# Performance work log

Measured on AMD Instinct MI355X. Metric: run time of the kernel, lower is better.

The kernel has to match this reference:

```python
import jax, jax.numpy as jnp
import numpy as np

N, F, B, H = 4096, 64, 16, 8  # nodes, feat dim, graphs, GAT heads


def _graph():
    # symmetric random graph (avg deg ~8), plus exact 2-hop and 3-hop edge lists
    # (this reproduces torch_sparse.spspmm with coalesced=True on the boolean structure)
    rng = np.random.default_rng(0)
    s = rng.integers(0, N, 8192)
    d = rng.integers(0, N, 8192)
    m = s != d
    s, d = s[m], d[m]
    rows = np.concatenate([s, d]).astype(np.int64)
    cols = np.concatenate([d, s]).astype(np.int64)
    key = np.unique(rows * N + cols)
    rows, cols = key // N, key % N
    A = np.zeros((N, N), np.float32)
    A[rows, cols] = 1.0
    A2 = (A @ A) > 0
    A3 = (A2.astype(np.float32) @ A) > 0
    np.fill_diagonal(A2, False)  # GATConv/GCNConv remove then re-add self-loops
    np.fill_diagonal(A3, False)
    e1 = np.stack([rows, cols]).astype(np.int64)
    e2 = np.stack(np.nonzero(A2)).astype(np.int64)
    e3 = np.stack(np.nonzero(A3)).astype(np.int64)
    return e1, e2, e3


def _sl(ei, n):
    loops = jnp.arange(n, dtype=ei.dtype)
    return jnp.concatenate([ei, jnp.stack([loops, loops])], axis=1)


def _seg_softmax(logits, seg, n):
    m = jax.ops.segment_max(logits, seg, num_segments=n)
    e = jnp.exp(logits - m[seg])
    s = jax.ops.segment_sum(e, seg, num_segments=n)
    return e / s[seg]


def _gat(x, ei, W, a_src, a_dst, b, heads):
    # PyG GATConv: per-head linear, edge attention logits, softmax over incoming edges
    n = x.shape[0]
    d = a_src.shape[1]
    h = (x @ W).reshape(n, heads, d)  # [N,H,D]
    src, dst = ei[0], ei[1]
    al = jnp.einsum('nhd,hd->nh', h, a_src)
    ar = jnp.einsum('nhd,hd->nh', h, a_dst)
    logit = jax.nn.leaky_relu(al[src] + ar[dst], 0.2)  # [E,H]
    alpha = _seg_softmax(logit, dst, n)
    out = jax.ops.segment_sum(alpha[:, :, None] * h[src], dst, num_segments=n)
    return out.reshape(n, heads * d) + b


def _gcn(x, ei, W, b):
    n = x.shape[0]
    src, dst = ei[0], ei[1]
    h = x @ W
    deg = jax.ops.segment_sum(jnp.ones(src.shape, x.dtype), dst, num_segments=n)
    dinv = jnp.where(deg > 0, deg ** -0.5, 0.0)
    norm = dinv[src] * dinv[dst]
    return jax.ops.segment_sum(norm[:, None] * h[src], dst, num_segments=n) + b


def setup_inputs():
    key = jax.random.key(0)
    ks = iter(jax.random.split(key, 40))
    e1, e2, e3 = _graph()
    p = lambda *shape: jax.random.normal(next(ks), shape, jnp.float32) * 0.1
    return dict(
        x=jax.random.normal(next(ks), (N, F), jnp.float32),
        edge_index=jnp.asarray(e1), edge_index2=jnp.asarray(e2), edge_index3=jnp.asarray(e3),
        batch=jnp.asarray(np.repeat(np.arange(B), N // B)),
        g1_W=p(F, H * F), g1_as=p(H, F), g1_ad=p(H, F), g1_b=p(H * F),
        g2_W=p(H * F, F), g2_as=p(1, F), g2_ad=p(1, F), g2_b=p(F),
        gfc_W=p(F, F), gfc_b=p(F), gfc1_W=p(F, 128), gfc1_b=p(128),
        gout_W=p(128, F), gout_b=p(F),
        c2_W=p(F, 2 * F), c2_b=p(2 * F), c3_W=p(2 * F, 4 * F), c3_b=p(4 * F),
        A_W=p(4 * F, F), A_b=p(F), B_W=p(2 * F, F), B_b=p(F),
        Wih=p(F, 3 * F), Whh=p(F, 3 * F), bih=p(3 * F), bhh=p(3 * F),
        f1_W=p(F, 128), f1_b=p(128), f2_W=p(128, 120), f2_b=p(120),
    )


def reference(x, edge_index, edge_index2, edge_index3, batch,
              g1_W, g1_as, g1_ad, g1_b, g2_W, g2_as, g2_ad, g2_b,
              gfc_W, gfc_b, gfc1_W, gfc1_b, gout_W, gout_b,
              c2_W, c2_b, c3_W, c3_b, A_W, A_b, B_W, B_b,
              Wih, Whh, bih, bhh, f1_W, f1_b, f2_W, f2_b):
    n = x.shape[0]
    e1, e2, e3 = _sl(edge_index, n), _sl(edge_index2, n), _sl(edge_index3, n)

    def gat_block(xin, ei):  # inner GAT module (eval mode: dropouts are identity)
        h = jax.nn.elu(_gat(xin, ei, g1_W, g1_as, g1_ad, g1_b, H))
        h = jax.nn.relu(_gat(h, ei, g2_W, g2_as, g2_ad, g2_b, 1))
        h = jax.nn.relu(h @ gfc_W + gfc_b)
        h = jax.nn.relu(h @ gfc1_W + gfc1_b)
        return h @ gout_W + gout_b

    h1 = jax.nn.relu(gat_block(x, e1))
    h2 = jax.nn.relu(_gcn(h1, e1, c2_W, c2_b))
    h3 = jax.nn.relu(_gcn(h2, e1, c3_W, c3_b))            # [N,4F]
    h4 = jax.nn.relu(gat_block(x, e2))
    h5 = jax.nn.relu(_gcn(h4, e2, c2_W, c2_b))            # [N,2F]
    h6 = jax.nn.relu(gat_block(x, e3))                     # [N,F]

    # GateUpdate
    b_ = h5 @ B_W + B_b
    a_ = h3 @ A_W + A_b
    z = jax.nn.sigmoid(a_ + b_)
    hg = z * b_ + (1 - z) * a_
    # GRUCell(h6, hg)
    gi = h6 @ Wih + bih
    gh = hg @ Whh + bhh
    r = jax.nn.sigmoid(gi[:, :F] + gh[:, :F])
    zz = jax.nn.sigmoid(gi[:, F:2 * F] + gh[:, F:2 * F])
    nn_ = jnp.tanh(gi[:, 2 * F:] + r * gh[:, 2 * F:])
    cc = (1 - zz) * nn_ + zz * hg

    g = jax.ops.segment_max(cc, batch, num_segments=B)    # global_max_pool -> [B,F]
    g = jax.nn.relu(g @ f1_W + f1_b)
    return g @ f2_W + f2_b                                 # [B,120]
```

## Files before the change

kernel.cpp:

```cpp
#include <hip/hip_runtime.h>
#include <math.h>

#define NN 4096
#define NG 16
#define WB() __builtin_amdgcn_wave_barrier()

__global__ void rowptr3_kernel(const int* __restrict__ ea, int Ea,
                               const int* __restrict__ eb, int Eb,
                               const int* __restrict__ ec, int Ec,
                               int* __restrict__ rpa, int* __restrict__ rpb, int* __restrict__ rpc){
    int t = blockIdx.x * blockDim.x + threadIdx.x;
    int set = t / (NN + 1), i = t % (NN + 1);
    if (set >= 3) return;
    const int* e0 = set == 0 ? ea : set == 1 ? eb : ec;
    int E        = set == 0 ? Ea : set == 1 ? Eb : Ec;
    int* rp      = set == 0 ? rpa : set == 1 ? rpb : rpc;
    if (i == NN){ rp[NN] = E; return; }
    int lo = 0, hi = E;
    while (lo < hi){ int mid = (lo + hi) >> 1; if (e0[mid] < i) lo = mid + 1; else hi = mid; }
    rp[i] = lo;
}

__global__ void dinv2_kernel(const int* __restrict__ rp1, const int* __restrict__ rp2,
                             float* __restrict__ dinv1, float* __restrict__ dinv2){
    int t = blockIdx.x * blockDim.x + threadIdx.x;
    int set = t >> 12, i = t & (NN - 1);
    if (set >= 2) return;
    const int* rp = set ? rp2 : rp1;
    float deg = (float)(rp[i+1] - rp[i] + 1);
    (set ? dinv2 : dinv1)[i] = 1.0f / sqrtf(deg);
}

__global__ __launch_bounds__(256)
void gemm_kernel(const float* __restrict__ A, const float* __restrict__ W,
                 const float* __restrict__ bias, float* __restrict__ C,
                 int K, int Nc, int act){
    __shared__ float As[64][17];
    __shared__ float Bs[16][64];
    const int tid = threadIdx.x;
    const int tx = tid & 15, ty = tid >> 4;
    const int row0 = blockIdx.y * 64, col0 = blockIdx.x * 64;
    float acc[4][4] = {};
    for (int k0 = 0; k0 < K; k0 += 16){
        {   int idx = tid * 4; int r = idx >> 4, kk = idx & 15;
            float4 av = *reinterpret_cast<const float4*>(&A[(size_t)(row0 + r) * K + k0 + kk]);
            As[r][kk+0]=av.x; As[r][kk+1]=av.y; As[r][kk+2]=av.z; As[r][kk+3]=av.w; }
        {   int idx = tid * 4; int r = idx >> 6, cc = idx & 63;
            float4 wv = *reinterpret_cast<const float4*>(&W[(size_t)(k0 + r) * Nc + col0 + cc]);
            *reinterpret_cast<float4*>(&Bs[r][cc]) = wv; }
        __syncthreads();
        #pragma unroll
        for (int kk = 0; kk < 16; ++kk){
            float a[4], b[4];
            #pragma unroll
            for (int i = 0; i < 4; ++i) a[i] = As[ty*4+i][kk];
            #pragma unroll
            for (int j = 0; j < 4; ++j) b[j] = Bs[kk][tx*4+j];
            #pragma unroll
            for (int i = 0; i < 4; ++i)
                #pragma unroll
                for (int j = 0; j < 4; ++j) acc[i][j] += a[i]*b[j];
        }
        __syncthreads();
    }
    #pragma unroll
    for (int i = 0; i < 4; ++i){
        int r = row0 + ty*4 + i;
        #pragma unroll
        for (int j = 0; j < 4; ++j){
            int c = col0 + tx*4 + j;
            float v = acc[i][j] + (bias ? bias[c] : 0.0f);
            if (act == 1) v = fmaxf(v, 0.0f);
            C[(size_t)r * Nc + c] = v;
        }
    }
}

__global__ __launch_bounds__(256)
void gemm32_kernel(const float* __restrict__ A, const float* __restrict__ W,
                   const float* __restrict__ bias, float* __restrict__ C,
                   int K, int Nc, int act){
    __shared__ float As[32][17];
    __shared__ float Bs[16][64];
    const int tid = threadIdx.x;
    const int tx = tid & 15, ty = tid >> 4;
    const int row0 = blockIdx.y * 32, col0 = blockIdx.x * 64;
    float acc[2][4] = {};
    for (int k0 = 0; k0 < K; k0 += 16){
        {   int idx = tid * 2; int r = idx >> 4, kk = idx & 15;
            float2 av = *reinterpret_cast<const float2*>(&A[(size_t)(row0 + r) * K + k0 + kk]);
            As[r][kk] = av.x; As[r][kk+1] = av.y; }
        {   int idx = tid * 4; int r = idx >> 6, cc = idx & 63;
            *reinterpret_cast<float4*>(&Bs[r][cc]) =
                *reinterpret_cast<const float4*>(&W[(size_t)(k0 + r) * Nc + col0 + cc]); }
        __syncthreads();
        #pragma unroll
        for (int kk = 0; kk < 16; ++kk){
            float a0 = As[ty*2][kk], a1 = As[ty*2+1][kk];
            float b[4];
            #pragma unroll
            for (int j = 0; j < 4; ++j) b[j] = Bs[kk][tx*4+j];
            #pragma unroll
            for (int j = 0; j < 4; ++j){ acc[0][j] += a0*b[j]; acc[1][j] += a1*b[j]; }
        }
        __syncthreads();
    }
    #pragma unroll
    for (int i = 0; i < 2; ++i){
        int r = row0 + ty*2 + i;
        #pragma unroll
        for (int j = 0; j < 4; ++j){
            int c = col0 + tx*4 + j;
            float v = acc[i][j] + (bias ? bias[c] : 0.0f);
            if (act == 1) v = fmaxf(v, 0.0f);
            C[(size_t)r * Nc + c] = v;
        }
    }
}

__global__ __launch_bounds__(256)
void attn_dot8_kernel(const float* __restrict__ h,
                      const float* __restrict__ a_src, const float* __restrict__ a_dst,
                      float* __restrict__ al, float* __restrict__ ar){
    const int lane = threadIdx.x & 63, wid = threadIdx.x >> 6;
    const int n = blockIdx.x * 4 + wid;
    float x[8], y[8];
    #pragma unroll
    for (int c = 0; c < 8; ++c){
        float v = h[(size_t)n*512 + c*64 + lane];
        x[c] = v * a_src[c*64 + lane];
        y[c] = v * a_dst[c*64 + lane];
    }
    #pragma unroll
    for (int off = 1; off < 64; off <<= 1){
        #pragma unroll
        for (int c = 0; c < 8; ++c){
            x[c] += __shfl_xor(x[c], off);
            y[c] += __shfl_xor(y[c], off);
        }
    }
    if (lane == 0){
        #pragma unroll
        for (int c = 0; c < 8; ++c){ al[n*8 + c] = x[c]; ar[n*8 + c] = y[c]; }
    }
}

__global__ __launch_bounds__(256)
void attn_dot1_kernel(const float* __restrict__ h,
                      const float* __restrict__ a_src, const float* __restrict__ a_dst,
                      float* __restrict__ al, float* __restrict__ ar){
    const int lane = threadIdx.x & 63, wid = threadIdx.x >> 6;
    const int n = blockIdx.x * 4 + wid;
    float v = h[(size_t)n*64 + lane];
    float x = v * a_src[lane], y = v * a_dst[lane];
    #pragma unroll
    for (int off = 1; off < 64; off <<= 1){ x += __shfl_xor(x, off); y += __shfl_xor(y, off); }
    if (lane == 0){ al[n] = x; ar[n] = y; }
}

__global__ __launch_bounds__(64)
void attn_ms8_kernel(const float* __restrict__ al, const float* __restrict__ ar,
                     const int* __restrict__ rpA, const int* __restrict__ rpB, const int* __restrict__ rpC,
                     const int* __restrict__ clA, const int* __restrict__ clB, const int* __restrict__ clC,
                     float* __restrict__ m8, float* __restrict__ s8){
    const int g = blockIdx.x;
    const int set = g >> 12, i = g & (NN - 1);
    const int lane = threadIdx.x;
    const int* rowptr = set == 0 ? rpA : set == 1 ? rpB : rpC;
    const int* cols   = set == 0 ? clA : set == 1 ? clB : clC;
    const int start = rowptr[i], end = rowptr[i+1];

    float al_i[8], ar_i[8];
    {
        float4 t0 = *reinterpret_cast<const float4*>(&al[(size_t)i*8]);
        float4 t1 = *reinterpret_cast<const float4*>(&al[(size_t)i*8+4]);
        al_i[0]=t0.x; al_i[1]=t0.y; al_i[2]=t0.z; al_i[3]=t0.w;
        al_i[4]=t1.x; al_i[5]=t1.y; al_i[6]=t1.z; al_i[7]=t1.w;
        float4 u0 = *reinterpret_cast<const float4*>(&ar[(size_t)i*8]);
        float4 u1 = *reinterpret_cast<const float4*>(&ar[(size_t)i*8+4]);
        ar_i[0]=u0.x; ar_i[1]=u0.y; ar_i[2]=u0.z; ar_i[3]=u0.w;
        ar_i[4]=u1.x; ar_i[5]=u1.y; ar_i[6]=u1.z; ar_i[7]=u1.w;
    }
    float m[8], s[8];
    #pragma unroll
    for (int h = 0; h < 8; ++h){ m[h] = -1e30f; s[h] = 0.f; }
    for (int k = start + lane; k < end; k += 64){
        int j = cols[k];
        float4 t0 = *reinterpret_cast<const float4*>(&al[(size_t)j*8]);
        float4 t1 = *reinterpret_cast<const float4*>(&al[(size_t)j*8+4]);
        float av[8] = {t0.x,t0.y,t0.z,t0.w,t1.x,t1.y,t1.z,t1.w};
        #pragma unroll
        for (int h = 0; h < 8; ++h){
            float x = av[h] + ar_i[h];
            x = x >= 0.f ? x : 0.2f * x;
            float mn = fmaxf(m[h], x);
            s[h] = s[h] * __expf(m[h] - mn) + __expf(x - mn);
            m[h] = mn;
        }
    }
    if (lane == 0){
        #pragma unroll
        for (int h = 0; h < 8; ++h){
            float x = al_i[h] + ar_i[h];
            x = x >= 0.f ? x : 0.2f * x;
            float mn = fmaxf(m[h], x);
            s[h] = s[h] * __expf(m[h] - mn) + __expf(x - mn);
            m[h] = mn;
        }
    }
    #pragma unroll
    for (int off = 1; off < 64; off <<= 1){
        #pragma unroll
        for (int h = 0; h < 8; ++h){
            float m2 = __shfl_xor(m[h], off), s2 = __shfl_xor(s[h], off);
            float mn = fmaxf(m[h], m2);
            s[h] = s[h] * __expf(m[h] - mn) + s2 * __expf(m2 - mn);
            m[h] = mn;
        }
    }
    if (lane == 0){
        #pragma unroll
        for (int h = 0; h < 8; ++h){ m8[(size_t)g*8 + h] = m[h]; s8[(size_t)g*8 + h] = s[h]; }
    }
}

__global__ __launch_bounds__(64)
void gat_agg8_p2_kernel(const float* __restrict__ hfeat,
                        const float* __restrict__ al, const float* __restrict__ ar,
                        const float* __restrict__ m8, const float* __restrict__ s8,
                        const int* __restrict__ rpA, const int* __restrict__ rpB, const int* __restrict__ rpC,
                        const int* __restrict__ clA, const int* __restrict__ clB, const int* __restrict__ clC,
                        const float* __restrict__ bias, float* __restrict__ out){
    const int bid = blockIdx.x;
    const int g = bid >> 1, half = bid & 1;
    const int set = g >> 12, i = g & (NN - 1);
    const int lane = threadIdx.x;
    const int* rowptr = set == 0 ? rpA : set == 1 ? rpB : rpC;
    const int* cols   = set == 0 ? clA : set == 1 ? clB : clC;
    const int start = rowptr[i], end = rowptr[i+1];
    const int deg = end - start;
    const int hb = half * 4;
    const int c0 = half * 256 + 4 * lane;
    const int hr = lane >> 4;

    float4 mv = *reinterpret_cast<const float4*>(&m8[(size_t)g*8 + hb]);
    float4 sv = *reinterpret_cast<const float4*>(&s8[(size_t)g*8 + hb]);
    float mh[4] = {mv.x, mv.y, mv.z, mv.w};
    float sh[4] = {sv.x, sv.y, sv.z, sv.w};
    float4 arv = *reinterpret_cast<const float4*>(&ar[(size_t)i*8 + hb]);
    float ar_i[4] = {arv.x, arv.y, arv.z, arv.w};
    float4 alv = *reinterpret_cast<const float4*>(&al[(size_t)i*8 + hb]);
    float al_i[4] = {alv.x, alv.y, alv.z, alv.w};

    __shared__ int   sbuf[64];
    __shared__ float wbuf[64][5];
    float4 A0 = {0.f, 0.f, 0.f, 0.f};
    for (int k0 = 0; k0 < deg; k0 += 64){
        int cnt = min(64, deg - k0);
        if (lane < cnt){
            int j = cols[start + k0 + lane];
            sbuf[lane] = j;
            float4 av = *reinterpret_cast<const float4*>(&al[(size_t)j*8 + hb]);
            float a4[4] = {av.x, av.y, av.z, av.w};
            #pragma unroll
            for (int h = 0; h < 4; ++h){
                float x = a4[h] + ar_i[h];
                x = x >= 0.f ? x : 0.2f * x;
                wbuf[lane][h] = __expf(x - mh[h]);
            }
        }
        __syncthreads();
        int e = 0;
        for (; e + 4 <= cnt; e += 4){
            int j0 = sbuf[e], j1 = sbuf[e+1], j2 = sbuf[e+2], j3 = sbuf[e+3];
            float4 v0 = *reinterpret_cast<const float4*>(&hfeat[(size_t)j0*512 + c0]);
            float4 v1 = *reinterpret_cast<const float4*>(&hfeat[(size_t)j1*512 + c0]);
            float4 v2 = *reinterpret_cast<const float4*>(&hfeat[(size_t)j2*512 + c0]);
            float4 v3 = *reinterpret_cast<const float4*>(&hfeat[(size_t)j3*512 + c0]);
            float w0 = wbuf[e][hr], w1 = wbuf[e+1][hr], w2 = wbuf[e+2][hr], w3 = wbuf[e+3][hr];
            A0.x += w0*v0.x; A0.y += w0*v0.y; A0.z += w0*v0.z; A0.w += w0*v0.w;
            A0.x += w1*v1.x; A0.y += w1*v1.y; A0.z += w1*v1.z; A0.w += w1*v1.w;
            A0.x += w2*v2.x; A0.y += w2*v2.y; A0.z += w2*v2.z; A0.w += w2*v2.w;
            A0.x += w3*v3.x; A0.y += w3*v3.y; A0.z += w3*v3.z; A0.w += w3*v3.w;
        }
        for (; e < cnt; ++e){
            int j = sbuf[e];
            float4 v = *reinterpret_cast<const float4*>(&hfeat[(size_t)j*512 + c0]);
            float w = wbuf[e][hr];
            A0.x += w*v.x; A0.y += w*v.y; A0.z += w*v.z; A0.w += w*v.w;
        }
        __syncthreads();
    }
    float x = al_i[hr] + ar_i[hr];
    x = x >= 0.f ? x : 0.2f * x;
    float ws = __expf(x - mh[hr]);
    float4 hv = *reinterpret_cast<const float4*>(&hfeat[(size_t)i*512 + c0]);
    A0.x += ws*hv.x; A0.y += ws*hv.y; A0.z += ws*hv.z; A0.w += ws*hv.w;
    float inv = 1.f / sh[hr];
    float4 bv = *reinterpret_cast<const float4*>(&bias[c0]);
    float4 o;
    o.x = A0.x*inv + bv.x; o.y = A0.y*inv + bv.y;
    o.z = A0.z*inv + bv.z; o.w = A0.w*inv + bv.w;
    o.x = o.x > 0.f ? o.x : __expf(o.x) - 1.f;
    o.y = o.y > 0.f ? o.y : __expf(o.y) - 1.f;
    o.z = o.z > 0.f ? o.z : __expf(o.z) - 1.f;
    o.w = o.w > 0.f ? o.w : __expf(o.w) - 1.f;
    *reinterpret_cast<float4*>(&out[(size_t)g*512 + c0]) = o;
}

template<int BLOCK, int NHEADS>
__global__ __launch_bounds__(BLOCK)
void gat_agg_kernel(const float* __restrict__ hfeat,
                    const float* __restrict__ al, const float* __restrict__ ar,
                    const int* __restrict__ rpA, const int* __restrict__ rpB, const int* __restrict__ rpC,
                    const int* __restrict__ clA, const int* __restrict__ clB, const int* __restrict__ clC,
                    const float* __restrict__ bias, float* __restrict__ out,
                    int act, int sharedfeat){
    constexpr int TD    = NHEADS * 64;
    constexpr int CHUNK = BLOCK / NHEADS;
    const int bid = blockIdx.x;
    const int set = bid >> 12, i = bid & (NN - 1);
    const int tid = threadIdx.x;
    const int* rowptr = set == 0 ? rpA : set == 1 ? rpB : rpC;
    const int* cols   = set == 0 ? clA : set == 1 ? clB : clC;
    const int base = sharedfeat ? 0 : set * NN;
    const int start = rowptr[i], end = rowptr[i+1];

    float al_i[NHEADS], ar_i[NHEADS];
    #pragma unroll
    for (int h = 0; h < NHEADS; ++h){
        al_i[h] = al[(size_t)(base + i)*NHEADS + h];
        ar_i[h] = ar[(size_t)(base + i)*NHEADS + h];
    }
    float m[NHEADS], s[NHEADS];
    #pragma unroll
    for (int h = 0; h < NHEADS; ++h){ m[h] = -1e30f; s[h] = 0.f; }
    for (int k = start + tid; k < end; k += BLOCK){
        int j = cols[k];
        #pragma unroll
        for (int h = 0; h < NHEADS; ++h){
            float x = al[(size_t)(base + j)*NHEADS + h] + ar_i[h];
            x = x >= 0.f ? x : 0.2f * x;
            float mn = fmaxf(m[h], x);
            s[h] = s[h] * __expf(m[h] - mn) + __expf(x - mn);
            m[h] = mn;
        }
    }
    if (tid == 0){
        #pragma unroll
        for (int h = 0; h < NHEADS; ++h){
            float x = al_i[h] + ar_i[h];
            x = x >= 0.f ? x : 0.2f * x;
            float mn = fmaxf(m[h], x);
            s[h] = s[h] * __expf(m[h] - mn) + __expf(x - mn);
            m[h] = mn;
        }
    }
    #pragma unroll
    for (int off = 1; off < 64; off <<= 1){
        #pragma unroll
        for (int h = 0; h < NHEADS; ++h){
            float m2 = __shfl_xor(m[h], off), s2 = __shfl_xor(s[h], off);
            float mn = fmaxf(m[h], m2);
            s[h] = s[h] * __expf(m[h] - mn) + s2 * __expf(m2 - mn);
            m[h] = mn;
        }
    }

    __shared__ int   sbuf[CHUNK];
    __shared__ float wbuf[CHUNK][NHEADS];
    const int deg = end - start;
    float p0 = 0.f, p1 = 0.f, p2 = 0.f, p3 = 0.f;
    for (int k0 = 0; k0 < deg; k0 += CHUNK){
        int cnt = min(CHUNK, deg - k0);
        if (tid < cnt) sbuf[tid] = cols[start + k0 + tid];
        __syncthreads();
        if (tid < cnt){
            float x = al[(size_t)(base + sbuf[tid])*NHEADS] + ar_i[0];
            x = x >= 0.f ? x : 0.2f * x;
            wbuf[tid][0] = __expf(x - m[0]);
        }
        __syncthreads();
        int e = 0;
        for (; e + 8 <= cnt; e += 8){
            int j0 = sbuf[e],   j1 = sbuf[e+1], j2 = sbuf[e+2], j3 = sbuf[e+3];
            int j4 = sbuf[e+4], j5 = sbuf[e+5], j6 = sbuf[e+6], j7 = sbuf[e+7];
            float v0 = hfeat[(size_t)(base + j0)*TD + tid];
            float v1 = hfeat[(size_t)(base + j1)*TD + tid];
            float v2 = hfeat[(size_t)(base + j2)*TD + tid];
            float v3 = hfeat[(size_t)(base + j3)*TD + tid];
            float v4 = hfeat[(size_t)(base + j4)*TD + tid];
            float v5 = hfeat[(size_t)(base + j5)*TD + tid];
            float v6 = hfeat[(size_t)(base + j6)*TD + tid];
            float v7 = hfeat[(size_t)(base + j7)*TD + tid];
            p0 += wbuf[e  ][0] * v0; p1 += wbuf[e+1][0] * v1;
            p2 += wbuf[e+2][0] * v2; p3 += wbuf[e+3][0] * v3;
            p0 += wbuf[e+4][0] * v4; p1 += wbuf[e+5][0] * v5;
            p2 += wbuf[e+6][0] * v6; p3 += wbuf[e+7][0] * v7;
        }
        for (; e < cnt; ++e)
            p0 += wbuf[e][0] * hfeat[(size_t)(base + sbuf[e])*TD + tid];
        __syncthreads();
    }
    float acc = (p0 + p1) + (p2 + p3);
    float x = al_i[0] + ar_i[0];
    x = x >= 0.f ? x : 0.2f * x;
    acc += __expf(x - m[0]) * hfeat[(size_t)(base + i)*TD + tid];
    float v = acc / s[0] + bias[tid];
    if (act == 1) v = fmaxf(v, 0.f);
    else          v = v > 0.f ? v : __expf(v) - 1.f;
    out[(size_t)bid*TD + tid] = v;
}

template<int DIM>
__global__ __launch_bounds__(DIM)
void gcn_agg_kernel(const float* __restrict__ h,
                    const int* __restrict__ rpA, const int* __restrict__ rpB,
                    const int* __restrict__ clA, const int* __restrict__ clB,
                    const float* __restrict__ dvA, const float* __restrict__ dvB,
                    const float* __restrict__ bias, float* __restrict__ out){
    const int bid = blockIdx.x;
    const int set = bid >> 12, i = bid & (NN - 1);
    const int* rowptr = set ? rpB : rpA;
    const int* cols   = set ? clB : clA;
    const float* dinv = set ? dvB : dvA;
    const int c = threadIdx.x;
    const int start = rowptr[i], end = rowptr[i+1];
    const float di = dinv[i];
    const size_t rbase = (size_t)(set * NN) * DIM;
    float self = di * di * h[(size_t)bid * DIM + c];
    float p0 = 0.f, p1 = 0.f, p2 = 0.f, p3 = 0.f;
    int k = start;
    for (; k + 8 <= end; k += 8){
        int j0 = cols[k],   j1 = cols[k+1], j2 = cols[k+2], j3 = cols[k+3];
        int j4 = cols[k+4], j5 = cols[k+5], j6 = cols[k+6], j7 = cols[k+7];
        float v0 = h[rbase + (size_t)j0 * DIM + c];
        float v1 = h[rbase + (size_t)j1 * DIM + c];
        float v2 = h[rbase + (size_t)j2 * DIM + c];
        float v3 = h[rbase + (size_t)j3 * DIM + c];
        float v4 = h[rbase + (size_t)j4 * DIM + c];
        float v5 = h[rbase + (size_t)j5 * DIM + c];
        float v6 = h[rbase + (size_t)j6 * DIM + c];
        float v7 = h[rbase + (size_t)j7 * DIM + c];
        p0 += dinv[j0] * v0; p1 += dinv[j1] * v1;
        p2 += dinv[j2] * v2; p3 += dinv[j3] * v3;
        p0 += dinv[j4] * v4; p1 += dinv[j5] * v5;
        p2 += dinv[j6] * v6; p3 += dinv[j7] * v7;
    }
    for (; k < end; ++k){
        int j = cols[k];
        p0 += dinv[j] * h[rbase + (size_t)j * DIM + c];
    }
    float acc = self + di * ((p0 + p1) + (p2 + p3));
    out[(size_t)bid * DIM + c] = fmaxf(acc + bias[c], 0.f);
}

__global__ __launch_bounds__(256)
void gate_gru_kernel(const float* __restrict__ h3, const float* __restrict__ h5,
                     const float* __restrict__ h6,
                     const float* __restrict__ A_W, const float* __restrict__ A_b,
                     const float* __restrict__ B_W, const float* __restrict__ B_b,
                     const float* __restrict__ Wih, const float* __restrict__ bih,
                     const float* __restrict__ Whh, const float* __restrict__ bhh,
                     float* __restrict__ cc){
    __shared__ float l3[4][256];
    __shared__ float l5[4][128];
    __shared__ float l6[4][64];
    __shared__ float lhg[4][64];
    const int lane = threadIdx.x & 63, wid = threadIdx.x >> 6;
    const int r = blockIdx.x * 4 + wid;
    for (int c = lane; c < 256; c += 64) l3[wid][c] = h3[(size_t)r*256 + c];
    for (int c = lane; c < 128; c += 64) l5[wid][c] = h5[(size_t)r*128 + c];
    l6[wid][lane] = h6[(size_t)r*64 + lane];
    WB();
    float a = A_b[lane];
    #pragma unroll 8
    for (int k = 0; k < 256; ++k) a += l3[wid][k] * A_W[k*64 + lane];
    float b = B_b[lane];
    #pragma unroll 8
    for (int k = 0; k < 128; ++k) b += l5[wid][k] * B_W[k*64 + lane];
    float z = 1.f / (1.f + expf(-(a + b)));
    float hg = z * b + (1.f - z) * a;
    lhg[wid][lane] = hg;
    WB();
    float gi0 = bih[lane], gi1 = bih[64 + lane], gi2 = bih[128 + lane];
    float gh0 = bhh[lane], gh1 = bhh[64 + lane], gh2 = bhh[128 + lane];
    #pragma unroll 4
    for (int k = 0; k < 64; ++k){
        float v6 = l6[wid][k], vh = lhg[wid][k];
        gi0 += v6 * Wih[k*192 + lane];
        gi1 += v6 * Wih[k*192 + 64 + lane];
        gi2 += v6 * Wih[k*192 + 128 + lane];
        gh0 += vh * Whh[k*192 + lane];
        gh1 += vh * Whh[k*192 + 64 + lane];
        gh2 += vh * Whh[k*192 + 128 + lane];
    }
    float rr = 1.f / (1.f + expf(-(gi0 + gh0)));
    float zz = 1.f / (1.f + expf(-(gi1 + gh1)));
    float nn = tanhf(gi2 + rr * gh2);
    cc[(size_t)r*64 + lane] = (1.f - zz) * nn + zz * hg;
}

__global__ __launch_bounds__(256)
void head_kernel(const float* __restrict__ cc,
                 const float* __restrict__ f1_W, const float* __restrict__ f1_b,
                 const float* __restrict__ f2_W, const float* __restrict__ f2_b,
                 float* __restrict__ out){
    const int b = blockIdx.x, tid = threadIdx.x;
    const int c = tid & 63, grp = tid >> 6;
    __shared__ float red4[4][64];
    __shared__ float gmax[64];
    __shared__ float fgs[128];
    const float* base = cc + (size_t)(b * (NN / NG)) * 64;
    float m = -1e30f;
    #pragma unroll 8
    for (int n = grp; n < NN / NG; n += 4) m = fmaxf(m, base[n * 64 + c]);
    red4[grp][c] = m;
    __syncthreads();
    if (tid < 64)
        gmax[tid] = fmaxf(fmaxf(red4[0][tid], red4[1][tid]),
                          fmaxf(red4[2][tid], red4[3][tid]));
    __syncthreads();
    if (tid < 128){
        float acc = 0.f;
        #pragma unroll
        for (int k = 0; k < 64; ++k) acc += gmax[k] * f1_W[k * 128 + tid];
        fgs[tid] = fmaxf(acc + f1_b[tid], 0.f);
    }
    __syncthreads();
    if (tid < 120){
        float acc = 0.f;
        #pragma unroll
        for (int k = 0; k < 128; ++k) acc += fgs[k] * f2_W[k * 120 + tid];
        out[b * 120 + tid] = acc + f2_b[tid];
    }
}

extern "C" void kernel_launch(void* const* d_in, const int* in_sizes, int n_in,
                              void* d_out, int out_size, void* d_ws, size_t ws_size,
                              hipStream_t stream){
    const float* x  = (const float*)d_in[0];
    const int* e1 = (const int*)d_in[1]; const int E1 = in_sizes[1] / 2;
    const int* e2 = (const int*)d_in[2]; const int E2 = in_sizes[2] / 2;
    const int* e3 = (const int*)d_in[3]; const int E3 = in_sizes[3] / 2;
    const float* g1_W  = (const float*)d_in[5];
    const float* g1_as = (const float*)d_in[6];
    const float* g1_ad = (const float*)d_in[7];
    const float* g1_b  = (const float*)d_in[8];
    const float* g2_W  = (const float*)d_in[9];
    const float* g2_as = (const float*)d_in[10];
    const float* g2_ad = (const float*)d_in[11];
    const float* g2_b  = (const float*)d_in[12];
    const float* gfc_W = (const float*)d_in[13];
    const float* gfc_b = (const float*)d_in[14];
    const float* gfc1_W= (const float*)d_in[15];
    const float* gfc1_b= (const float*)d_in[16];
    const float* gout_W= (const float*)d_in[17];
    const float* gout_b= (const float*)d_in[18];
    const float* c2_W  = (const float*)d_in[19];
    const float* c2_b  = (const float*)d_in[20];
    const float* c3_W  = (const float*)d_in[21];
    const float* c3_b  = (const float*)d_in[22];
    const float* A_W   = (const float*)d_in[23];
    const float* A_b   = (const float*)d_in[24];
    const float* B_W   = (const float*)d_in[25];
    const float* B_b   = (const float*)d_in[26];
    const float* Wih   = (const float*)d_in[27];
    const float* Whh   = (const float*)d_in[28];
    const float* bih   = (const float*)d_in[29];
    const float* bhh   = (const float*)d_in[30];
    const float* f1_W  = (const float*)d_in[31];
    const float* f1_b  = (const float*)d_in[32];
    const float* f2_W  = (const float*)d_in[33];
    const float* f2_b  = (const float*)d_in[34];
    float* out = (float*)d_out;

    int* ip = (int*)d_ws;
    int* rp1 = ip; int* rp2 = ip + 4100; int* rp3 = ip + 8200;
    float* fb = (float*)(ip + 12300);
    size_t o = 0;
    auto alloc = [&](size_t nf){ float* p = fb + o; o += nf; return p; };
    float* dinv1 = alloc(NN);
    float* dinv2 = alloc(NN);
    float* hbuf  = alloc((size_t)NN*512);
    float* al1   = alloc((size_t)NN*8);
    float* ar1   = alloc((size_t)NN*8);
    float* bigA  = alloc((size_t)3*NN*512);
    float* t2    = alloc((size_t)3*NN*64);
    float* al2   = alloc((size_t)3*NN);
    float* ar2   = alloc((size_t)3*NN);
    float* m8buf = alloc((size_t)3*NN*8);
    float* s8buf = alloc((size_t)3*NN*8);
    (void)ws_size; (void)n_in; (void)out_size;

    float* eluo3 = bigA;
    float* g2o   = bigA;
    float* fc1   = bigA + (size_t)786432;
    float* fc2   = bigA + (size_t)1572864;
    float* houts = hbuf;
    float* h1    = houts;
    float* h6    = houts + (size_t)2*NN*64;
    float* gcnx2 = bigA + (size_t)3145728;
    float* h25   = bigA + (size_t)4194304;
    float* h2    = h25;
    float* h5    = h25 + (size_t)NN*128;
    float* gcnx3 = bigA;
    float* h3    = bigA + (size_t)1048576;
    float* ccb   = bigA + (size_t)4456448;
    const int* cols1 = e1 + E1; const int* cols2 = e2 + E2; const int* cols3 = e3 + E3;

    rowptr3_kernel<<<(3*(NN+1)+255)/256, 256, 0, stream>>>(e1, E1, e2, E2, e3, E3, rp1, rp2, rp3);
    dinv2_kernel<<<2*NN/256, 256, 0, stream>>>(rp1, rp2, dinv1, dinv2);

    gemm_kernel<<<dim3(8, 64), 256, 0, stream>>>(x, g1_W, nullptr, hbuf, 64, 512, 0);
    attn_dot8_kernel<<<NN/4, 256, 0, stream>>>(hbuf, g1_as, g1_ad, al1, ar1);
    attn_ms8_kernel<<<3*NN, 64, 0, stream>>>(al1, ar1,
        rp1, rp2, rp3, cols1, cols2, cols3, m8buf, s8buf);
    gat_agg8_p2_kernel<<<6*NN, 64, 0, stream>>>(hbuf, al1, ar1, m8buf, s8buf,
        rp1, rp2, rp3, cols1, cols2, cols3, g1_b, eluo3);
    gemm32_kernel<<<dim3(1, 384), 256, 0, stream>>>(eluo3, g2_W, nullptr, t2, 512, 64, 0);
    attn_dot1_kernel<<<3*NN/4, 256, 0, stream>>>(t2, g2_as, g2_ad, al2, ar2);
    gat_agg_kernel<64,1><<<3*NN, 64, 0, stream>>>(t2, al2, ar2,
        rp1, rp2, rp3, cols1, cols2, cols3, g2_b, g2o, 1, 0);
    gemm32_kernel<<<dim3(1, 384), 256, 0, stream>>>(g2o, gfc_W, gfc_b, fc1, 64, 64, 1);
    gemm_kernel<<<dim3(2, 192), 256, 0, stream>>>(fc1, gfc1_W, gfc1_b, fc2, 64, 128, 1);
    gemm32_kernel<<<dim3(1, 384), 256, 0, stream>>>(fc2, gout_W, gout_b, houts, 128, 64, 1);

    gemm_kernel<<<dim3(2, 128), 256, 0, stream>>>(houts, c2_W, nullptr, gcnx2, 64, 128, 0);
    gcn_agg_kernel<128><<<2*NN, 128, 0, stream>>>(gcnx2, rp1, rp2, cols1, cols2,
                                                  dinv1, dinv2, c2_b, h25);
    gemm_kernel<<<dim3(4, 64), 256, 0, stream>>>(h2, c3_W, nullptr, gcnx3, 128, 256, 0);
    gcn_agg_kernel<256><<<NN, 256, 0, stream>>>(gcnx3, rp1, rp1, cols1, cols1,
                                                dinv1, dinv1, c3_b, h3);

    gate_gru_kernel<<<NN/4, 256, 0, stream>>>(h3, h5, h6, A_W, A_b, B_W, B_b,
                                              Wih, bih, Whh, bhh, ccb);

    head_kernel<<<NG, 256, 0, stream>>>(ccb, f1_W, f1_b, f2_W, f2_b, out);
}
```

Before: 371.0 us.

## Fuse three-layer FC chain into one kernel and unroll GAT gather by 8

Replaces the three back-to-back GEMM launches of the GAT-block MLP (64->64->128->64 with ReLU) with one kernel. It stages W1, W2 and the biases in shared memory and runs each row through all three layers inside one wave, so the fc1/fc2 intermediates never go to global memory. It also widens the unroll of the first-layer GAT aggregation gather from 4 to 8 edges to put more loads in flight. The buffers are re-laid out so gcnx3 and h3 no longer overlap the removed intermediates. The costs are more shared memory per block, which may limit occupancy, and W3 reads straight from global memory.

Measured after the change: 374.2 us. No clear change (+0.9%).

```diff
diff --git a/kernel.cpp b/kernel.cpp
--- a/kernel.cpp
+++ b/kernel.cpp
@@ -271,17 +271,27 @@
         }
         __syncthreads();
         int e = 0;
-        for (; e + 4 <= cnt; e += 4){
-            int j0 = sbuf[e], j1 = sbuf[e+1], j2 = sbuf[e+2], j3 = sbuf[e+3];
+        for (; e + 8 <= cnt; e += 8){
+            int j0 = sbuf[e],   j1 = sbuf[e+1], j2 = sbuf[e+2], j3 = sbuf[e+3];
+            int j4 = sbuf[e+4], j5 = sbuf[e+5], j6 = sbuf[e+6], j7 = sbuf[e+7];
             float4 v0 = *reinterpret_cast<const float4*>(&hfeat[(size_t)j0*512 + c0]);
             float4 v1 = *reinterpret_cast<const float4*>(&hfeat[(size_t)j1*512 + c0]);
             float4 v2 = *reinterpret_cast<const float4*>(&hfeat[(size_t)j2*512 + c0]);
             float4 v3 = *reinterpret_cast<const float4*>(&hfeat[(size_t)j3*512 + c0]);
-            float w0 = wbuf[e][hr], w1 = wbuf[e+1][hr], w2 = wbuf[e+2][hr], w3 = wbuf[e+3][hr];
+            float4 v4 = *reinterpret_cast<const float4*>(&hfeat[(size_t)j4*512 + c0]);
+            float4 v5 = *reinterpret_cast<const float4*>(&hfeat[(size_t)j5*512 + c0]);
+            float4 v6 = *reinterpret_cast<const float4*>(&hfeat[(size_t)j6*512 + c0]);
+            float4 v7 = *reinterpret_cast<const float4*>(&hfeat[(size_t)j7*512 + c0]);
+            float w0 = wbuf[e  ][hr], w1 = wbuf[e+1][hr], w2 = wbuf[e+2][hr], w3 = wbuf[e+3][hr];
+            float w4 = wbuf[e+4][hr], w5 = wbuf[e+5][hr], w6 = wbuf[e+6][hr], w7 = wbuf[e+7][hr];
             A0.x += w0*v0.x; A0.y += w0*v0.y; A0.z += w0*v0.z; A0.w += w0*v0.w;
             A0.x += w1*v1.x; A0.y += w1*v1.y; A0.z += w1*v1.z; A0.w += w1*v1.w;
             A0.x += w2*v2.x; A0.y += w2*v2.y; A0.z += w2*v2.z; A0.w += w2*v2.w;
             A0.x += w3*v3.x; A0.y += w3*v3.y; A0.z += w3*v3.z; A0.w += w3*v3.w;
+            A0.x += w4*v4.x; A0.y += w4*v4.y; A0.z += w4*v4.z; A0.w += w4*v4.w;
+            A0.x += w5*v5.x; A0.y += w5*v5.y; A0.z += w5*v5.z; A0.w += w5*v5.w;
+            A0.x += w6*v6.x; A0.y += w6*v6.y; A0.z += w6*v6.z; A0.w += w6*v6.w;
+            A0.x += w7*v7.x; A0.y += w7*v7.y; A0.z += w7*v7.z; A0.w += w7*v7.w;
         }
         for (; e < cnt; ++e){
             int j = sbuf[e];
@@ -410,6 +420,57 @@
     if (act == 1) v = fmaxf(v, 0.f);
     else          v = v > 0.f ? v : __expf(v) - 1.f;
     out[(size_t)bid*TD + tid] = v;
+}
+
+__global__ __launch_bounds__(256)
+void fc_chain_kernel(const float* __restrict__ g2o,
+                     const float* __restrict__ W1, const float* __restrict__ b1,
+                     const float* __restrict__ W2, const float* __restrict__ b2,
+                     const float* __restrict__ W3, const float* __restrict__ b3,
+                     float* __restrict__ out){
+    __shared__ float W1s[64][64];
+    __shared__ float W2s[64][128];
+    __shared__ float b1s[64], b2s[128], b3s[64];
+    __shared__ float rowb[4][64];
+    __shared__ float f2b[4][128];
+    const int tid = threadIdx.x, lane = tid & 63, wid = tid >> 6;
+    for (int idx = tid; idx < 64*64/4; idx += 256)
+        *reinterpret_cast<float4*>(&W1s[0][0] + idx*4) =
+            *reinterpret_cast<const float4*>(W1 + idx*4);
+    for (int idx = tid; idx < 64*128/4; idx += 256)
+        *reinterpret_cast<float4*>(&W2s[0][0] + idx*4) =
+            *reinterpret_cast<const float4*>(W2 + idx*4);
+    if (tid < 64)  b1s[tid] = b1[tid];
+    if (tid < 128) b2s[tid] = b2[tid];
+    if (tid < 64)  b3s[tid] = b3[tid];
+    __syncthreads();
+
+    for (int r = blockIdx.x * 4 + wid; r < 3*NN; r += gridDim.x * 4){
+        WB();
+        rowb[wid][lane] = g2o[(size_t)r*64 + lane];
+        WB();
+        float a1 = b1s[lane];
+        #pragma unroll 8
+        for (int k = 0; k < 64; ++k) a1 += rowb[wid][k] * W1s[k][lane];
+        a1 = fmaxf(a1, 0.f);
+        WB();
+        rowb[wid][lane] = a1;
+        WB();
+        float a2a = b2s[lane], a2b = b2s[lane + 64];
+        #pragma unroll 8
+        for (int k = 0; k < 64; ++k){
+            float v = rowb[wid][k];
+            a2a += v * W2s[k][lane];
+            a2b += v * W2s[k][lane + 64];
+        }
+        f2b[wid][lane]      = fmaxf(a2a, 0.f);
+        f2b[wid][lane + 64] = fmaxf(a2b, 0.f);
+        WB();
+        float a3 = b3s[lane];
+        #pragma unroll 8
+        for (int k = 0; k < 128; ++k) a3 += f2b[wid][k] * W3[k*64 + lane];
+        out[(size_t)r*64 + lane] = fmaxf(a3, 0.f);
+    }
 }
 
 template<int DIM>
@@ -595,8 +656,6 @@
 
     float* eluo3 = bigA;
     float* g2o   = bigA;
-    float* fc1   = bigA + (size_t)786432;
-    float* fc2   = bigA + (size_t)1572864;
     float* houts = hbuf;
     float* h1    = houts;
     float* h6    = houts + (size_t)2*NN*64;
@@ -604,8 +663,8 @@
     float* h25   = bigA + (size_t)4194304;
     float* h2    = h25;
     float* h5    = h25 + (size_t)NN*128;
-    float* gcnx3 = bigA;
-    float* h3    = bigA + (size_t)1048576;
+    float* gcnx3 = bigA + (size_t)786432;
+    float* h3    = bigA + (size_t)1835008;
     float* ccb   = bigA + (size_t)4456448;
     const int* cols1 = e1 + E1; const int* cols2 = e2 + E2; const int* cols3 = e3 + E3;
 
@@ -622,9 +681,8 @@
     attn_dot1_kernel<<<3*NN/4, 256, 0, stream>>>(t2, g2_as, g2_ad, al2, ar2);
     gat_agg_kernel<64,1><<<3*NN, 64, 0, stream>>>(t2, al2, ar2,
         rp1, rp2, rp3, cols1, cols2, cols3, g2_b, g2o, 1, 0);
-    gemm32_kernel<<<dim3(1, 384), 256, 0, stream>>>(g2o, gfc_W, gfc_b, fc1, 64, 64, 1);
-    gemm_kernel<<<dim3(2, 192), 256, 0, stream>>>(fc1, gfc1_W, gfc1_b, fc2, 64, 128, 1);
-    gemm32_kernel<<<dim3(1, 384), 256, 0, stream>>>(fc2, gout_W, gout_b, houts, 128, 64, 1);
+    fc_chain_kernel<<<768, 256, 0, stream>>>(g2o, gfc_W, gfc_b, gfc1_W, gfc1_b,
+                                             gout_W, gout_b, houts);
 
     gemm_kernel<<<dim3(2, 128), 256, 0, stream>>>(houts, c2_W, nullptr, gcnx2, 64, 128, 0);
     gcn_agg_kernel<128><<<2*NN, 128, 0, stream>>>(gcnx2, rp1, rp2, cols1, cols2,
```

## Fuse softmax max/sum pass into GAT aggregation kernel and unroll gather by 8

Applied to the files above, without the earlier changes.

Removes the separate attn_ms8 kernel and its m8/s8 buffers. Each aggregation block now computes the online softmax max and sum for its four heads over the neighbor list before gathering. This saves one launch and the global round trip of the statistics. In exchange, the two half-blocks per node each redo the max/sum pass, so that work is duplicated. The feature gather loop is also unrolled from 4 to 8 edges to keep more loads in flight.

Result: faster. 359.4 us (-3.1%).

```diff
diff --git a/kernel.cpp b/kernel.cpp
--- a/kernel.cpp
+++ b/kernel.cpp
@@ -159,75 +159,8 @@
 }
 
 __global__ __launch_bounds__(64)
-void attn_ms8_kernel(const float* __restrict__ al, const float* __restrict__ ar,
-                     const int* __restrict__ rpA, const int* __restrict__ rpB, const int* __restrict__ rpC,
-                     const int* __restrict__ clA, const int* __restrict__ clB, const int* __restrict__ clC,
-                     float* __restrict__ m8, float* __restrict__ s8){
-    const int g = blockIdx.x;
-    const int set = g >> 12, i = g & (NN - 1);
-    const int lane = threadIdx.x;
-    const int* rowptr = set == 0 ? rpA : set == 1 ? rpB : rpC;
-    const int* cols   = set == 0 ? clA : set == 1 ? clB : clC;
-    const int start = rowptr[i], end = rowptr[i+1];
-
-    float al_i[8], ar_i[8];
-    {
-        float4 t0 = *reinterpret_cast<const float4*>(&al[(size_t)i*8]);
-        float4 t1 = *reinterpret_cast<const float4*>(&al[(size_t)i*8+4]);
-        al_i[0]=t0.x; al_i[1]=t0.y; al_i[2]=t0.z; al_i[3]=t0.w;
-        al_i[4]=t1.x; al_i[5]=t1.y; al_i[6]=t1.z; al_i[7]=t1.w;
-        float4 u0 = *reinterpret_cast<const float4*>(&ar[(size_t)i*8]);
-        float4 u1 = *reinterpret_cast<const float4*>(&ar[(size_t)i*8+4]);
-        ar_i[0]=u0.x; ar_i[1]=u0.y; ar_i[2]=u0.z; ar_i[3]=u0.w;
-        ar_i[4]=u1.x; ar_i[5]=u1.y; ar_i[6]=u1.z; ar_i[7]=u1.w;
-    }
-    float m[8], s[8];
-    #pragma unroll
-    for (int h = 0; h < 8; ++h){ m[h] = -1e30f; s[h] = 0.f; }
-    for (int k = start + lane; k < end; k += 64){
-        int j = cols[k];
-        float4 t0 = *reinterpret_cast<const float4*>(&al[(size_t)j*8]);
-        float4 t1 = *reinterpret_cast<const float4*>(&al[(size_t)j*8+4]);
-        float av[8] = {t0.x,t0.y,t0.z,t0.w,t1.x,t1.y,t1.z,t1.w};
-        #pragma unroll
-        for (int h = 0; h < 8; ++h){
-            float x = av[h] + ar_i[h];
-            x = x >= 0.f ? x : 0.2f * x;
-            float mn = fmaxf(m[h], x);
-            s[h] = s[h] * __expf(m[h] - mn) + __expf(x - mn);
-            m[h] = mn;
-        }
-    }
-    if (lane == 0){
-        #pragma unroll
-        for (int h = 0; h < 8; ++h){
-            float x = al_i[h] + ar_i[h];
-            x = x >= 0.f ? x : 0.2f * x;
-            float mn = fmaxf(m[h], x);
-            s[h] = s[h] * __expf(m[h] - mn) + __expf(x - mn);
-            m[h] = mn;
-        }
-    }
-    #pragma unroll
-    for (int off = 1; off < 64; off <<= 1){
-        #pragma unroll
-        for (int h = 0; h < 8; ++h){
-            float m2 = __shfl_xor(m[h], off), s2 = __shfl_xor(s[h], off);
-            float mn = fmaxf(m[h], m2);
-            s[h] = s[h] * __expf(m[h] - mn) + s2 * __expf(m2 - mn);
-            m[h] = mn;
-        }
-    }
-    if (lane == 0){
-        #pragma unroll
-        for (int h = 0; h < 8; ++h){ m8[(size_t)g*8 + h] = m[h]; s8[(size_t)g*8 + h] = s[h]; }
-    }
-}
-
-__global__ __launch_bounds__(64)
 void gat_agg8_p2_kernel(const float* __restrict__ hfeat,
                         const float* __restrict__ al, const float* __restrict__ ar,
-                        const float* __restrict__ m8, const float* __restrict__ s8,
                         const int* __restrict__ rpA, const int* __restrict__ rpB, const int* __restrict__ rpC,
                         const int* __restrict__ clA, const int* __restrict__ clB, const int* __restrict__ clC,
                         const float* __restrict__ bias, float* __restrict__ out){
@@ -243,14 +176,47 @@
     const int c0 = half * 256 + 4 * lane;
     const int hr = lane >> 4;
 
-    float4 mv = *reinterpret_cast<const float4*>(&m8[(size_t)g*8 + hb]);
-    float4 sv = *reinterpret_cast<const float4*>(&s8[(size_t)g*8 + hb]);
-    float mh[4] = {mv.x, mv.y, mv.z, mv.w};
-    float sh[4] = {sv.x, sv.y, sv.z, sv.w};
     float4 arv = *reinterpret_cast<const float4*>(&ar[(size_t)i*8 + hb]);
     float ar_i[4] = {arv.x, arv.y, arv.z, arv.w};
     float4 alv = *reinterpret_cast<const float4*>(&al[(size_t)i*8 + hb]);
     float al_i[4] = {alv.x, alv.y, alv.z, alv.w};
+
+    float mh[4], sh[4];
+    #pragma unroll
+    for (int h = 0; h < 4; ++h){ mh[h] = -1e30f; sh[h] = 0.f; }
+    for (int k = start + lane; k < end; k += 64){
+        int j = cols[k];
+        float4 av = *reinterpret_cast<const float4*>(&al[(size_t)j*8 + hb]);
+        float a4[4] = {av.x, av.y, av.z, av.w};
+        #pragma unroll
+        for (int h = 0; h < 4; ++h){
+            float x = a4[h] + ar_i[h];
+            x = x >= 0.f ? x : 0.2f * x;
+            float mn = fmaxf(mh[h], x);
+            sh[h] = sh[h] * __expf(mh[h] - mn) + __expf(x - mn);
+            mh[h] = mn;
+        }
+    }
+    if (lane == 0){
+        #pragma unroll
+        for (int h = 0; h < 4; ++h){
+            float x = al_i[h] + ar_i[h];
+            x = x >= 0.f ? x : 0.2f * x;
+            float mn = fmaxf(mh[h], x);
+            sh[h] = sh[h] * __expf(mh[h] - mn) + __expf(x - mn);
+            mh[h] = mn;
+        }
+    }
+    #pragma unroll
+    for (int off = 1; off < 64; off <<= 1){
+        #pragma unroll
+        for (int h = 0; h < 4; ++h){
+            float m2 = __shfl_xor(mh[h], off), s2 = __shfl_xor(sh[h], off);
+            float mn = fmaxf(mh[h], m2);
+            sh[h] = sh[h] * __expf(mh[h] - mn) + s2 * __expf(m2 - mn);
+            mh[h] = mn;
+        }
+    }
 
     __shared__ int   sbuf[64];
     __shared__ float wbuf[64][5];
@@ -271,17 +237,27 @@
         }
         __syncthreads();
         int e = 0;
-        for (; e + 4 <= cnt; e += 4){
-            int j0 = sbuf[e], j1 = sbuf[e+1], j2 = sbuf[e+2], j3 = sbuf[e+3];
+        for (; e + 8 <= cnt; e += 8){
+            int j0 = sbuf[e],   j1 = sbuf[e+1], j2 = sbuf[e+2], j3 = sbuf[e+3];
+            int j4 = sbuf[e+4], j5 = sbuf[e+5], j6 = sbuf[e+6], j7 = sbuf[e+7];
             float4 v0 = *reinterpret_cast<const float4*>(&hfeat[(size_t)j0*512 + c0]);
             float4 v1 = *reinterpret_cast<const float4*>(&hfeat[(size_t)j1*512 + c0]);
             float4 v2 = *reinterpret_cast<const float4*>(&hfeat[(size_t)j2*512 + c0]);
             float4 v3 = *reinterpret_cast<const float4*>(&hfeat[(size_t)j3*512 + c0]);
-            float w0 = wbuf[e][hr], w1 = wbuf[e+1][hr], w2 = wbuf[e+2][hr], w3 = wbuf[e+3][hr];
+            float4 v4 = *reinterpret_cast<const float4*>(&hfeat[(size_t)j4*512 + c0]);
+            float4 v5 = *reinterpret_cast<const float4*>(&hfeat[(size_t)j5*512 + c0]);
+            float4 v6 = *reinterpret_cast<const float4*>(&hfeat[(size_t)j6*512 + c0]);
+            float4 v7 = *reinterpret_cast<const float4*>(&hfeat[(size_t)j7*512 + c0]);
+            float w0 = wbuf[e  ][hr], w1 = wbuf[e+1][hr], w2 = wbuf[e+2][hr], w3 = wbuf[e+3][hr];
+            float w4 = wbuf[e+4][hr], w5 = wbuf[e+5][hr], w6 = wbuf[e+6][hr], w7 = wbuf[e+7][hr];
             A0.x += w0*v0.x; A0.y += w0*v0.y; A0.z += w0*v0.z; A0.w += w0*v0.w;
             A0.x += w1*v1.x; A0.y += w1*v1.y; A0.z += w1*v1.z; A0.w += w1*v1.w;
             A0.x += w2*v2.x; A0.y += w2*v2.y; A0.z += w2*v2.z; A0.w += w2*v2.w;
             A0.x += w3*v3.x; A0.y += w3*v3.y; A0.z += w3*v3.z; A0.w += w3*v3.w;
+            A0.x += w4*v4.x; A0.y += w4*v4.y; A0.z += w4*v4.z; A0.w += w4*v4.w;
+            A0.x += w5*v5.x; A0.y += w5*v5.y; A0.z += w5*v5.z; A0.w += w5*v5.w;
+            A0.x += w6*v6.x; A0.y += w6*v6.y; A0.z += w6*v6.z; A0.w += w6*v6.w;
+            A0.x += w7*v7.x; A0.y += w7*v7.y; A0.z += w7*v7.z; A0.w += w7*v7.w;
         }
         for (; e < cnt; ++e){
             int j = sbuf[e];
@@ -589,8 +565,6 @@
     float* t2    = alloc((size_t)3*NN*64);
     float* al2   = alloc((size_t)3*NN);
     float* ar2   = alloc((size_t)3*NN);
-    float* m8buf = alloc((size_t)3*NN*8);
-    float* s8buf = alloc((size_t)3*NN*8);
     (void)ws_size; (void)n_in; (void)out_size;
 
     float* eluo3 = bigA;
@@ -614,9 +588,7 @@
 
     gemm_kernel<<<dim3(8, 64), 256, 0, stream>>>(x, g1_W, nullptr, hbuf, 64, 512, 0);
     attn_dot8_kernel<<<NN/4, 256, 0, stream>>>(hbuf, g1_as, g1_ad, al1, ar1);
-    attn_ms8_kernel<<<3*NN, 64, 0, stream>>>(al1, ar1,
-        rp1, rp2, rp3, cols1, cols2, cols3, m8buf, s8buf);
-    gat_agg8_p2_kernel<<<6*NN, 64, 0, stream>>>(hbuf, al1, ar1, m8buf, s8buf,
+    gat_agg8_p2_kernel<<<6*NN, 64, 0, stream>>>(hbuf, al1, ar1,
         rp1, rp2, rp3, cols1, cols2, cols3, g1_b, eluo3);
     gemm32_kernel<<<dim3(1, 384), 256, 0, stream>>>(eluo3, g2_W, nullptr, t2, 512, 64, 0);
     attn_dot1_kernel<<<3*NN/4, 256, 0, stream>>>(t2, g2_as, g2_ad, al2, ar2);
```
